# Kernel tuning notes

Hardware: AMD Instinct MI355X
Metric: run time of the kernel (lower is better)

The kernel has to match this reference:

```python
import jax, jax.numpy as jnp
import numpy as np
import math

B, T, D = 4, 2048, 1024
NHEAD = 16
HEAD_DIM = D // NHEAD
MAX_REL = 16  # max_relative_position default


def setup_inputs() -> dict:
    key = jax.random.key(0)
    ks = jax.random.split(key, 10)
    s = 1.0 / math.sqrt(D)
    inp = {
        "x": jax.random.normal(ks[0], (B, T, D), dtype=jnp.float32),
        "Wq": jax.random.normal(ks[1], (D, D), dtype=jnp.float32) * s,
        "bq": jnp.zeros((D,), dtype=jnp.float32),
        "Wk": jax.random.normal(ks[2], (D, D), dtype=jnp.float32) * s,
        "bk": jnp.zeros((D,), dtype=jnp.float32),
        "Wv": jax.random.normal(ks[3], (D, D), dtype=jnp.float32) * s,
        "bv": jnp.zeros((D,), dtype=jnp.float32),
        "rel_bias": jax.random.normal(ks[4], (2 * MAX_REL - 1, NHEAD), dtype=jnp.float32) * 0.02,
        "Wo": jax.random.normal(ks[5], (D, D), dtype=jnp.float32) * s,
        "bo": jnp.zeros((D,), dtype=jnp.float32),
    }
    return inp


def _relative_bias(rel_bias, seq_len):
    # distance matrix clamped to [-(MAX_REL-1), MAX_REL-1], shifted to index table
    r = jnp.arange(seq_len)
    dist = jnp.clip(r[None, :] - r[:, None], -MAX_REL + 1, MAX_REL - 1) + MAX_REL - 1
    # gather: [T, T, H] -> [H, T, T]
    return jnp.transpose(rel_bias[dist], (2, 0, 1))


def reference(x, Wq, bq, Wk, bk, Wv, bv, rel_bias, Wo, bo):
    Bdim, Tdim, Ddim = x.shape
    # torch Linear: x @ W.T + b
    Q = x @ Wq.T + bq
    K = x @ Wk.T + bk
    V = x @ Wv.T + bv
    # [B, H, T, hd]
    Q = Q.reshape(Bdim, Tdim, NHEAD, HEAD_DIM).transpose(0, 2, 1, 3)
    K = K.reshape(Bdim, Tdim, NHEAD, HEAD_DIM).transpose(0, 2, 1, 3)
    V = V.reshape(Bdim, Tdim, NHEAD, HEAD_DIM).transpose(0, 2, 1, 3)
    scores = jnp.einsum("bhqd,bhkd->bhqk", Q, K) / math.sqrt(HEAD_DIM)
    scores = scores + _relative_bias(rel_bias, Tdim)[None]  # [1,H,T,T]
    attn = jax.nn.softmax(scores, axis=-1)
    out = jnp.einsum("bhqk,bhkd->bhqd", attn, V)
    out = out.transpose(0, 2, 1, 3).reshape(Bdim, Tdim, Ddim)
    return out @ Wo.T + bo
```

## Files before the change

kernel.cpp:

```cpp
#include <hip/hip_runtime.h>
#include <stdint.h>
#include <math.h>

typedef unsigned short u16;
typedef __bf16 bf16x8 __attribute__((ext_vector_type(8)));
typedef float f32x4 __attribute__((ext_vector_type(4)));
typedef float f32x2 __attribute__((ext_vector_type(2)));
typedef unsigned short u16x8 __attribute__((ext_vector_type(8)));
typedef unsigned short u16x4 __attribute__((ext_vector_type(4)));

#define BATCH 4
#define SEQT 2048
#define DMODEL 1024
#define NHEAD 16
#define HDIM 64
#define LOG2E 1.44269504f

#define LDS_GLD16(gp, lp)                                                     \
  __builtin_amdgcn_global_load_lds(                                           \
      (const __attribute__((address_space(1))) void*)(gp),                    \
      (__attribute__((address_space(3))) void*)(lp), 16, 0, 0)

static __device__ __forceinline__ u16 f2bf(float f) {
  union { float f; uint32_t u; } c; c.f = f;
  uint32_t u = c.u;
  return (u16)((u + 0x7fffu + ((u >> 16) & 1u)) >> 16);
}
static __device__ __forceinline__ u16 f2bf_fast(float f) {
  union { float f; uint32_t u; } c; c.f = f;
  return (u16)((c.u + 0x8000u) >> 16);
}
static __device__ __forceinline__ uint32_t pkbf(float a, float b) {
  union { float f; uint32_t u; } ca, cb; ca.f = a; cb.f = b;
  return __builtin_amdgcn_perm(cb.u + 0x8000u, ca.u + 0x8000u, 0x07060302u);
}

__global__ __launch_bounds__(256) void k_convert_all(
    const float* __restrict__ x, const float* __restrict__ Wq,
    const float* __restrict__ Wk, const float* __restrict__ Wv,
    const float* __restrict__ Wo, u16* __restrict__ xbf,
    u16* __restrict__ Wqkv, u16* __restrict__ Wob) {
  const int NX4 = 2097152, NW4 = 262144;
  int i = blockIdx.x * 256 + threadIdx.x;
  const float* s; u16* d; int js, jd;
  if (i < NX4) {
    s = x; d = xbf; js = jd = i;
  } else if (i < NX4 + 3 * NW4) {
    int j = i - NX4;
    int w = j >> 18;
    s = (w == 0) ? Wq : (w == 1) ? Wk : Wv;
    js = j & (NW4 - 1);
    d = Wqkv; jd = j;
  } else {
    s = Wo; d = Wob; js = jd = i - NX4 - 3 * NW4;
  }
  float4 v = ((const float4*)s)[js];
  u16x4 o = {f2bf(v.x), f2bf(v.y), f2bf(v.z), f2bf(v.w)};
  ((u16x4*)d)[jd] = o;
}

__global__ __launch_bounds__(256) void k_gemm_qk(
    const u16* __restrict__ A, const u16* __restrict__ Bqk,
    const float* __restrict__ bq_, const float* __restrict__ bk_,
    u16* __restrict__ dq, u16* __restrict__ dk) {
  __shared__ u16 As[128 * 64];
  __shared__ u16 Bs[128 * 64];

  const int tid = threadIdx.x;
  const int wave = tid >> 6, lane = tid & 63;
  const int quad = lane >> 4, l16 = lane & 15;
  const int wm = wave & 1, wn = wave >> 1;
  const int m0 = blockIdx.x * 128, n0 = blockIdx.y * 128;
  const int lrow = lane >> 3, lcol = (lane & 7) * 8;

  f32x4 acc[4][4] = {};

  for (int kt = 0; kt < 1024; kt += 64) {
    __syncthreads();
    for (int c = 0; c < 4; ++c) {
      int rr = (wave * 4 + c) * 8 + lrow;
      LDS_GLD16(A + (size_t)(m0 + rr) * 1024 + kt + lcol,
                &As[(wave * 4 + c) * 512]);
      LDS_GLD16(Bqk + (size_t)(n0 + rr) * 1024 + kt + lcol,
                &Bs[(wave * 4 + c) * 512]);
    }
    __syncthreads();
    for (int kh = 0; kh < 2; ++kh) {
      bf16x8 af[4], bfr[4];
      for (int mt = 0; mt < 4; ++mt)
        af[mt] = *(const bf16x8*)&As[(wm * 64 + mt * 16 + l16) * 64 + kh * 32 +
                                     quad * 8];
      for (int nt = 0; nt < 4; ++nt)
        bfr[nt] = *(const bf16x8*)&Bs[(wn * 64 + nt * 16 + l16) * 64 + kh * 32 +
                                      quad * 8];
      for (int mt = 0; mt < 4; ++mt)
        for (int nt = 0; nt < 4; ++nt)
          acc[mt][nt] = __builtin_amdgcn_mfma_f32_16x16x32_bf16(
              af[mt], bfr[nt], acc[mt][nt], 0, 0, 0);
    }
  }

  u16* dst = (n0 < 1024) ? dq : dk;
  const float* bias = (n0 < 1024) ? bq_ : bk_;
  for (int mt = 0; mt < 4; ++mt)
    for (int nt = 0; nt < 4; ++nt) {
      int nn = (n0 + wn * 64 + nt * 16 + l16) & 1023;
      float bv = bias[nn];
      int h = nn >> 6, hd = nn & 63;
      for (int r = 0; r < 4; ++r) {
        int m = m0 + wm * 64 + mt * 16 + quad * 4 + r;
        int b = m >> 11, t = m & 2047;
        dst[(((size_t)b * NHEAD + h) * SEQT + t) * HDIM + hd] =
            f2bf_fast(acc[mt][nt][r] + bv);
      }
    }
}

__global__ __launch_bounds__(256) void k_gemm_vt(const u16* __restrict__ A,
                                                 const u16* __restrict__ Bx,
                                                 const float* __restrict__ bv_,
                                                 u16* __restrict__ Vt) {
  __shared__ u16 As[128 * 64];
  __shared__ u16 Bs[128 * 64];
  __shared__ float biasS[128];

  const int tid = threadIdx.x;
  const int wave = tid >> 6, lane = tid & 63;
  const int quad = lane >> 4, l16 = lane & 15;
  const int wm = wave & 1, wn = wave >> 1;
  const int m0 = blockIdx.x * 128, n0 = blockIdx.y * 128;
  const int lrow = lane >> 3, lcol = (lane & 7) * 8;

  if (tid < 128) biasS[tid] = bv_[m0 + tid];

  f32x4 acc[4][4] = {};

  for (int kt = 0; kt < 1024; kt += 64) {
    __syncthreads();
    for (int c = 0; c < 4; ++c) {
      int rr = (wave * 4 + c) * 8 + lrow;
      LDS_GLD16(A + (size_t)(m0 + rr) * 1024 + kt + lcol,
                &As[(wave * 4 + c) * 512]);
      LDS_GLD16(Bx + (size_t)(n0 + rr) * 1024 + kt + lcol,
                &Bs[(wave * 4 + c) * 512]);
    }
    __syncthreads();
    for (int kh = 0; kh < 2; ++kh) {
      bf16x8 af[4], bfr[4];
      for (int mt = 0; mt < 4; ++mt)
        af[mt] = *(const bf16x8*)&As[(wm * 64 + mt * 16 + l16) * 64 + kh * 32 +
                                     quad * 8];
      for (int nt = 0; nt < 4; ++nt)
        bfr[nt] = *(const bf16x8*)&Bs[(wn * 64 + nt * 16 + l16) * 64 + kh * 32 +
                                      quad * 8];
      for (int mt = 0; mt < 4; ++mt)
        for (int nt = 0; nt < 4; ++nt)
          acc[mt][nt] = __builtin_amdgcn_mfma_f32_16x16x32_bf16(
              af[mt], bfr[nt], acc[mt][nt], 0, 0, 0);
    }
  }

  for (int mt = 0; mt < 4; ++mt)
    for (int nt = 0; nt < 4; ++nt) {
      int n = n0 + wn * 64 + nt * 16 + l16;
      int b = n >> 11, t = n & 2047;
      for (int r = 0; r < 4; ++r) {
        int m = m0 + wm * 64 + mt * 16 + quad * 4 + r;
        float v = acc[mt][nt][r] + biasS[m - m0];
        Vt[((size_t)(b * NHEAD + (m >> 6)) * HDIM + (m & 63)) * SEQT + t] =
            f2bf_fast(v);
      }
    }
}

__global__ __launch_bounds__(256) void k_gemm_proj(const u16* __restrict__ A,
                                                   const u16* __restrict__ Bm,
                                                   const float* __restrict__ bias,
                                                   float* __restrict__ out) {
  __shared__ u16 As[128 * 64];
  __shared__ u16 Bs[128 * 64];

  const int tid = threadIdx.x;
  const int wave = tid >> 6, lane = tid & 63;
  const int quad = lane >> 4, l16 = lane & 15;
  const int wm = wave & 1, wn = wave >> 1;
  const int m0 = blockIdx.x * 128, n0 = blockIdx.y * 128;
  const int lrow = lane >> 3, lcol = (lane & 7) * 8;

  f32x4 acc[4][4] = {};

  for (int kt = 0; kt < 1024; kt += 64) {
    __syncthreads();
    for (int c = 0; c < 4; ++c) {
      int rr = (wave * 4 + c) * 8 + lrow;
      LDS_GLD16(A + (size_t)(m0 + rr) * 1024 + kt + lcol,
                &As[(wave * 4 + c) * 512]);
      LDS_GLD16(Bm + (size_t)(n0 + rr) * 1024 + kt + lcol,
                &Bs[(wave * 4 + c) * 512]);
    }
    __syncthreads();
    for (int kh = 0; kh < 2; ++kh) {
      bf16x8 af[4], bfr[4];
      for (int mt = 0; mt < 4; ++mt)
        af[mt] = *(const bf16x8*)&As[(wm * 64 + mt * 16 + l16) * 64 + kh * 32 +
                                     quad * 8];
      for (int nt = 0; nt < 4; ++nt)
        bfr[nt] = *(const bf16x8*)&Bs[(wn * 64 + nt * 16 + l16) * 64 + kh * 32 +
                                      quad * 8];
      for (int mt = 0; mt < 4; ++mt)
        for (int nt = 0; nt < 4; ++nt)
          acc[mt][nt] = __builtin_amdgcn_mfma_f32_16x16x32_bf16(
              af[mt], bfr[nt], acc[mt][nt], 0, 0, 0);
    }
  }

  for (int mt = 0; mt < 4; ++mt)
    for (int nt = 0; nt < 4; ++nt) {
      int n = n0 + wn * 64 + nt * 16 + l16;
      float bv = bias[n];
      for (int r = 0; r < 4; ++r) {
        int m = m0 + wm * 64 + mt * 16 + quad * 4 + r;
        out[(size_t)m * 1024 + n] = acc[mt][nt][r] + bv;
      }
    }
}

__global__ __launch_bounds__(512, 8) void k_attn(const u16* __restrict__ Qb,
                                                 const u16* __restrict__ Kb,
                                                 const u16* __restrict__ Vt,
                                                 const float* __restrict__ relb,
                                                 u16* __restrict__ Obf) {
  __shared__ u16 Ks[64 * 64];
  __shared__ u16 VTs[64 * 64];
  __shared__ u16 Ps[8][16 * 72];
  __shared__ float biasL[32];

  const int tid = threadIdx.x;
  const int wave = tid >> 6, lane = tid & 63;
  const int quad = lane >> 4, l16 = lane & 15;
  const int qt = blockIdx.x;
  const int bh = blockIdx.y;
  const int h = bh & (NHEAD - 1);
  const size_t base = (size_t)bh * SEQT * HDIM;
  const int q0 = qt * 128;
  const int qa = q0 + wave * 16;

  if (tid < 31) biasL[tid] = relb[tid * NHEAD + h] * LOG2E;
  const float bLo = relb[0 * NHEAD + h] * LOG2E;
  const float bHi = relb[30 * NHEAD + h] * LOG2E;
  const float CL = 0.125f * LOG2E;

  bf16x8 bq0, bq1;
  {
    const u16* qp = Qb + base + (size_t)(qa + l16) * HDIM;
    bq0 = *(const bf16x8*)(qp + quad * 8);
    bq1 = *(const bf16x8*)(qp + 32 + quad * 8);
  }

  f32x4 Oacc[4] = {};
  f32x2 ls2 = {};

  const int rl = lane >> 3;
  const int gb = (lane & 7) ^ rl;
  const int srow = wave * 8 + rl;
  const u16* kgp = Kb + base + (size_t)srow * HDIM + gb * 8;
  const u16* vgp = Vt + base + (size_t)srow * SEQT + gb * 8;
  u16* ksl = &Ks[wave * 512];
  u16* vsl = &VTs[wave * 512];
  const int sl = l16 & 7;

  for (int kt2 = 0; kt2 < 32; ++kt2) {
    const int k0 = kt2 * 64;
    __syncthreads();
    LDS_GLD16(kgp + (size_t)k0 * HDIM, ksl);
    LDS_GLD16(vgp + k0, vsl);
    __syncthreads();

    for (int kg = 0; kg < 4; ++kg) {
      const int krow = kg * 16 + l16;
      bf16x8 ak0 = *(const bf16x8*)&Ks[krow * 64 + ((quad ^ sl) << 3)];
      bf16x8 ak1 = *(const bf16x8*)&Ks[krow * 64 + (((4 + quad) ^ sl) << 3)];
      f32x4 s = {};
      s = __builtin_amdgcn_mfma_f32_16x16x32_bf16(ak0, bq0, s, 0, 0, 0);
      s = __builtin_amdgcn_mfma_f32_16x16x32_bf16(ak1, bq1, s, 0, 0, 0);
      const int kb = k0 + kg * 16;
      float p0, p1, p2, p3;
      const int dmin = kb - (qa + 15);
      const int dmax = kb + 15 - qa;
      if (dmin >= 15 || dmax <= -15) {
        const float ub = (dmin >= 15) ? bHi : bLo;
        p0 = __builtin_amdgcn_exp2f(fmaf(s[0], CL, ub));
        p1 = __builtin_amdgcn_exp2f(fmaf(s[1], CL, ub));
        p2 = __builtin_amdgcn_exp2f(fmaf(s[2], CL, ub));
        p3 = __builtin_amdgcn_exp2f(fmaf(s[3], CL, ub));
      } else {
        const int db = kb + quad * 4 - (qa + l16);
        float pv[4];
        for (int r = 0; r < 4; ++r) {
          int d = db + r;
          d = d < -15 ? -15 : (d > 15 ? 15 : d);
          pv[r] = __builtin_amdgcn_exp2f(fmaf(s[r], CL, biasL[d + 15]));
        }
        p0 = pv[0]; p1 = pv[1]; p2 = pv[2]; p3 = pv[3];
      }
      f32x2 t01 = {p0, p1}, t23 = {p2, p3};
      ls2 += t01 + t23;
      uint2 w;
      w.x = pkbf(p0, p1);
      w.y = pkbf(p2, p3);
      *(uint2*)&Ps[wave][l16 * 72 + kg * 16 + quad * 4] = w;
    }

    bf16x8 bp0 = *(const bf16x8*)&Ps[wave][l16 * 72 + quad * 8];
    bf16x8 bp1 = *(const bf16x8*)&Ps[wave][l16 * 72 + 32 + quad * 8];
    for (int dg = 0; dg < 4; ++dg) {
      const int d = dg * 16 + l16;
      bf16x8 av0 = *(const bf16x8*)&VTs[d * 64 + ((quad ^ sl) << 3)];
      bf16x8 av1 = *(const bf16x8*)&VTs[d * 64 + (((4 + quad) ^ sl) << 3)];
      Oacc[dg] = __builtin_amdgcn_mfma_f32_16x16x32_bf16(av0, bp0, Oacc[dg], 0, 0, 0);
      Oacc[dg] = __builtin_amdgcn_mfma_f32_16x16x32_bf16(av1, bp1, Oacc[dg], 0, 0, 0);
    }
  }

  float v = ls2.x + ls2.y;
  v += __shfl_xor(v, 16, 64);
  v += __shfl_xor(v, 32, 64);
  const float rinv = 1.0f / v;

  const int b = bh >> 4;
  const int t = qa + l16;
  u16* op = Obf + ((size_t)(b * SEQT + t)) * DMODEL + h * HDIM;
  for (int dg = 0; dg < 4; ++dg) {
    uint2 w;
    w.x = pkbf(Oacc[dg][0] * rinv, Oacc[dg][1] * rinv);
    w.y = pkbf(Oacc[dg][2] * rinv, Oacc[dg][3] * rinv);
    *(uint2*)(op + dg * 16 + quad * 4) = w;
  }
}

extern "C" void kernel_launch(void* const* d_in, const int* in_sizes, int n_in,
                              void* d_out, int out_size, void* d_ws,
                              size_t ws_size, hipStream_t stream) {
  const float* x = (const float*)d_in[0];
  const float* Wq = (const float*)d_in[1];
  const float* bq = (const float*)d_in[2];
  const float* Wk = (const float*)d_in[3];
  const float* bk = (const float*)d_in[4];
  const float* Wv = (const float*)d_in[5];
  const float* bv = (const float*)d_in[6];
  const float* relb = (const float*)d_in[7];
  const float* Wo = (const float*)d_in[8];
  const float* bo = (const float*)d_in[9];
  float* out = (float*)d_out;

  char* ws = (char*)d_ws;
  const size_t SZ_X = (size_t)BATCH * SEQT * DMODEL * 2;
  const size_t SZ_W = (size_t)DMODEL * DMODEL * 2;
  u16* xbf = (u16*)(ws);
  u16* Wqb = (u16*)(ws + SZ_X);
  u16* Wvb = (u16*)(ws + SZ_X + 2 * SZ_W);
  u16* Wob = (u16*)(ws + SZ_X + 3 * SZ_W);
  u16* Qb = (u16*)(ws + SZ_X + 4 * SZ_W);
  u16* Kb = (u16*)(ws + 2 * SZ_X + 4 * SZ_W);
  u16* Vt = (u16*)(ws + 3 * SZ_X + 4 * SZ_W);
  u16* Obf = (u16*)(ws + 4 * SZ_X + 4 * SZ_W);

  k_convert_all<<<12288, 256, 0, stream>>>(x, Wq, Wk, Wv, Wo, xbf, Wqb, Wob);
  k_gemm_qk<<<dim3(64, 16), 256, 0, stream>>>(xbf, Wqb, bq, bk, Qb, Kb);
  k_gemm_vt<<<dim3(8, 64), 256, 0, stream>>>(Wvb, xbf, bv, Vt);
  k_attn<<<dim3(16, 64), 512, 0, stream>>>(Qb, Kb, Vt, relb, Obf);
  k_gemm_proj<<<dim3(64, 8), 256, 0, stream>>>(Obf, Wob, bo, out);
}
```

Before: 323.1 us.

## Switch attention to 32x32x16 MFMA and keep P in registers

```diff
diff --git a/kernel.cpp b/kernel.cpp
--- a/kernel.cpp
+++ b/kernel.cpp
@@ -5,7 +5,7 @@
 typedef unsigned short u16;
 typedef __bf16 bf16x8 __attribute__((ext_vector_type(8)));
 typedef float f32x4 __attribute__((ext_vector_type(4)));
-typedef float f32x2 __attribute__((ext_vector_type(2)));
+typedef float f32x16 __attribute__((ext_vector_type(16)));
 typedef unsigned short u16x8 __attribute__((ext_vector_type(8)));
 typedef unsigned short u16x4 __attribute__((ext_vector_type(4)));
 
@@ -33,6 +33,12 @@
 static __device__ __forceinline__ uint32_t pkbf(float a, float b) {
   union { float f; uint32_t u; } ca, cb; ca.f = a; cb.f = b;
   return __builtin_amdgcn_perm(cb.u + 0x8000u, ca.u + 0x8000u, 0x07060302u);
+}
+static __device__ __forceinline__ bf16x8 mk_bf8(uint32_t x0, uint32_t x1,
+                                                uint32_t x2, uint32_t x3) {
+  union { uint32_t u[4]; bf16x8 v; } t;
+  t.u[0] = x0; t.u[1] = x1; t.u[2] = x2; t.u[3] = x3;
+  return t.v;
 }
 
 __global__ __launch_bounds__(256) void k_convert_all(
@@ -225,117 +231,123 @@
     }
 }
 
-__global__ __launch_bounds__(512, 8) void k_attn(const u16* __restrict__ Qb,
+__global__ __launch_bounds__(256, 4) void k_attn(const u16* __restrict__ Qb,
                                                  const u16* __restrict__ Kb,
                                                  const u16* __restrict__ Vt,
                                                  const float* __restrict__ relb,
                                                  u16* __restrict__ Obf) {
   __shared__ u16 Ks[64 * 64];
   __shared__ u16 VTs[64 * 64];
-  __shared__ u16 Ps[8][16 * 72];
   __shared__ float biasL[32];
 
   const int tid = threadIdx.x;
   const int wave = tid >> 6, lane = tid & 63;
-  const int quad = lane >> 4, l16 = lane & 15;
+  const int l32 = lane & 31, hi = lane >> 5;
   const int qt = blockIdx.x;
   const int bh = blockIdx.y;
   const int h = bh & (NHEAD - 1);
   const size_t base = (size_t)bh * SEQT * HDIM;
-  const int q0 = qt * 128;
-  const int qa = q0 + wave * 16;
+  const int qa = qt * 128 + wave * 32;
 
   if (tid < 31) biasL[tid] = relb[tid * NHEAD + h] * LOG2E;
   const float bLo = relb[0 * NHEAD + h] * LOG2E;
   const float bHi = relb[30 * NHEAD + h] * LOG2E;
   const float CL = 0.125f * LOG2E;
 
-  bf16x8 bq0, bq1;
+  bf16x8 bq[4];
   {
-    const u16* qp = Qb + base + (size_t)(qa + l16) * HDIM;
-    bq0 = *(const bf16x8*)(qp + quad * 8);
-    bq1 = *(const bf16x8*)(qp + 32 + quad * 8);
-  }
-
-  f32x4 Oacc[4] = {};
-  f32x2 ls2 = {};
-
-  const int rl = lane >> 3;
-  const int gb = (lane & 7) ^ rl;
-  const int srow = wave * 8 + rl;
-  const u16* kgp = Kb + base + (size_t)srow * HDIM + gb * 8;
-  const u16* vgp = Vt + base + (size_t)srow * SEQT + gb * 8;
-  u16* ksl = &Ks[wave * 512];
-  u16* vsl = &VTs[wave * 512];
-  const int sl = l16 & 7;
+    const u16* qp = Qb + base + (size_t)(qa + l32) * HDIM + hi * 8;
+    for (int ds = 0; ds < 4; ++ds) bq[ds] = *(const bf16x8*)(qp + ds * 16);
+  }
+
+  f32x16 Oacc[2] = {};
+  float ls = 0.f;
+
+  const int rl = lane >> 3, gb = lane & 7;
+  const int row0 = wave * 8 + rl, row1 = row0 + 32;
+  const u16* kgp0 = Kb + base + (size_t)row0 * HDIM + ((gb ^ (row0 & 7)) << 3);
+  const u16* kgp1 = Kb + base + (size_t)row1 * HDIM + ((gb ^ (row1 & 7)) << 3);
+  const u16* vgp0 = Vt + base + (size_t)row0 * SEQT + ((gb ^ (row0 & 7)) << 3);
+  const u16* vgp1 = Vt + base + (size_t)row1 * SEQT + ((gb ^ (row1 & 7)) << 3);
+  u16* ksl0 = &Ks[wave * 512 + lane * 8];
+  u16* ksl1 = ksl0 + 2048;
+  u16* vsl0 = &VTs[wave * 512 + lane * 8];
+  u16* vsl1 = vsl0 + 2048;
 
   for (int kt2 = 0; kt2 < 32; ++kt2) {
     const int k0 = kt2 * 64;
     __syncthreads();
-    LDS_GLD16(kgp + (size_t)k0 * HDIM, ksl);
-    LDS_GLD16(vgp + k0, vsl);
-    __syncthreads();
-
-    for (int kg = 0; kg < 4; ++kg) {
-      const int krow = kg * 16 + l16;
-      bf16x8 ak0 = *(const bf16x8*)&Ks[krow * 64 + ((quad ^ sl) << 3)];
-      bf16x8 ak1 = *(const bf16x8*)&Ks[krow * 64 + (((4 + quad) ^ sl) << 3)];
-      f32x4 s = {};
-      s = __builtin_amdgcn_mfma_f32_16x16x32_bf16(ak0, bq0, s, 0, 0, 0);
-      s = __builtin_amdgcn_mfma_f32_16x16x32_bf16(ak1, bq1, s, 0, 0, 0);
-      const int kb = k0 + kg * 16;
-      float p0, p1, p2, p3;
-      const int dmin = kb - (qa + 15);
-      const int dmax = kb + 15 - qa;
-      if (dmin >= 15 || dmax <= -15) {
+    LDS_GLD16(kgp0 + (size_t)k0 * HDIM, ksl0);
+    LDS_GLD16(kgp1 + (size_t)k0 * HDIM, ksl1);
+    LDS_GLD16(vgp0 + k0, vsl0);
+    LDS_GLD16(vgp1 + k0, vsl1);
+    __syncthreads();
+
+    for (int kgrp = 0; kgrp < 2; ++kgrp) {
+      const int kb = k0 + kgrp * 32;
+      f32x16 c = {};
+      for (int ds = 0; ds < 4; ++ds) {
+        const int key = kgrp * 32 + l32;
+        bf16x8 ak = *(const bf16x8*)&Ks[key * 64 +
+                                        (((ds * 2 + hi) ^ (key & 7)) << 3)];
+        c = __builtin_amdgcn_mfma_f32_32x32x16_bf16(ak, bq[ds], c, 0, 0, 0);
+      }
+
+      const int dmin = kb - (qa + 31);
+      if (dmin >= 15 || kb + 31 - qa <= -15) {
         const float ub = (dmin >= 15) ? bHi : bLo;
-        p0 = __builtin_amdgcn_exp2f(fmaf(s[0], CL, ub));
-        p1 = __builtin_amdgcn_exp2f(fmaf(s[1], CL, ub));
-        p2 = __builtin_amdgcn_exp2f(fmaf(s[2], CL, ub));
-        p3 = __builtin_amdgcn_exp2f(fmaf(s[3], CL, ub));
+        for (int i = 0; i < 16; ++i)
+          c[i] = __builtin_amdgcn_exp2f(fmaf(c[i], CL, ub));
       } else {
-        const int db = kb + quad * 4 - (qa + l16);
-        float pv[4];
-        for (int r = 0; r < 4; ++r) {
-          int d = db + r;
+        const int dbase = kb + 4 * hi - (qa + l32);
+        for (int i = 0; i < 16; ++i) {
+          int d = dbase + (i & 3) + 8 * (i >> 2);
           d = d < -15 ? -15 : (d > 15 ? 15 : d);
-          pv[r] = __builtin_amdgcn_exp2f(fmaf(s[r], CL, biasL[d + 15]));
+          c[i] = __builtin_amdgcn_exp2f(fmaf(c[i], CL, biasL[d + 15]));
         }
-        p0 = pv[0]; p1 = pv[1]; p2 = pv[2]; p3 = pv[3];
-      }
-      f32x2 t01 = {p0, p1}, t23 = {p2, p3};
-      ls2 += t01 + t23;
+      }
+      {
+        float s0 = (c[0] + c[1]) + (c[2] + c[3]);
+        float s1 = (c[4] + c[5]) + (c[6] + c[7]);
+        float s2 = (c[8] + c[9]) + (c[10] + c[11]);
+        float s3 = (c[12] + c[13]) + (c[14] + c[15]);
+        ls += (s0 + s1) + (s2 + s3);
+      }
+
+      uint32_t p[8];
+      for (int i = 0; i < 8; ++i) p[i] = pkbf(c[2 * i], c[2 * i + 1]);
+
+      for (int ks = 0; ks < 2; ++ks) {
+        bf16x8 bp = mk_bf8(p[ks * 4 + 0], p[ks * 4 + 1], p[ks * 4 + 2],
+                           p[ks * 4 + 3]);
+        const int blk = kgrp * 4 + ks * 2;
+        for (int dg = 0; dg < 2; ++dg) {
+          const int d = dg * 32 + l32;
+          const int sw = d & 7;
+          uint2 a0 = *(const uint2*)&VTs[d * 64 + ((blk ^ sw) << 3) + 4 * hi];
+          uint2 a1 =
+              *(const uint2*)&VTs[d * 64 + (((blk + 1) ^ sw) << 3) + 4 * hi];
+          bf16x8 av = mk_bf8(a0.x, a0.y, a1.x, a1.y);
+          Oacc[dg] = __builtin_amdgcn_mfma_f32_32x32x16_bf16(av, bp, Oacc[dg],
+                                                             0, 0, 0);
+        }
+      }
+    }
+  }
+
+  ls += __shfl_xor(ls, 32, 64);
+  const float rinv = 1.0f / ls;
+
+  const int b = bh >> 4;
+  const int t = qa + l32;
+  u16* op = Obf + ((size_t)(b * SEQT + t)) * DMODEL + h * HDIM;
+  for (int dg = 0; dg < 2; ++dg)
+    for (int a = 0; a < 4; ++a) {
       uint2 w;
-      w.x = pkbf(p0, p1);
-      w.y = pkbf(p2, p3);
-      *(uint2*)&Ps[wave][l16 * 72 + kg * 16 + quad * 4] = w;
-    }
-
-    bf16x8 bp0 = *(const bf16x8*)&Ps[wave][l16 * 72 + quad * 8];
-    bf16x8 bp1 = *(const bf16x8*)&Ps[wave][l16 * 72 + 32 + quad * 8];
-    for (int dg = 0; dg < 4; ++dg) {
-      const int d = dg * 16 + l16;
-      bf16x8 av0 = *(const bf16x8*)&VTs[d * 64 + ((quad ^ sl) << 3)];
-      bf16x8 av1 = *(const bf16x8*)&VTs[d * 64 + (((4 + quad) ^ sl) << 3)];
-      Oacc[dg] = __builtin_amdgcn_mfma_f32_16x16x32_bf16(av0, bp0, Oacc[dg], 0, 0, 0);
-      Oacc[dg] = __builtin_amdgcn_mfma_f32_16x16x32_bf16(av1, bp1, Oacc[dg], 0, 0, 0);
-    }
-  }
-
-  float v = ls2.x + ls2.y;
-  v += __shfl_xor(v, 16, 64);
-  v += __shfl_xor(v, 32, 64);
-  const float rinv = 1.0f / v;
-
-  const int b = bh >> 4;
-  const int t = qa + l16;
-  u16* op = Obf + ((size_t)(b * SEQT + t)) * DMODEL + h * HDIM;
-  for (int dg = 0; dg < 4; ++dg) {
-    uint2 w;
-    w.x = pkbf(Oacc[dg][0] * rinv, Oacc[dg][1] * rinv);
-    w.y = pkbf(Oacc[dg][2] * rinv, Oacc[dg][3] * rinv);
-    *(uint2*)(op + dg * 16 + quad * 4) = w;
-  }
+      w.x = pkbf(Oacc[dg][4 * a + 0] * rinv, Oacc[dg][4 * a + 1] * rinv);
+      w.y = pkbf(Oacc[dg][4 * a + 2] * rinv, Oacc[dg][4 * a + 3] * rinv);
+      *(uint2*)(op + dg * 32 + 8 * a + 4 * hi) = w;
+    }
 }
 
 extern "C" void kernel_launch(void* const* d_in, const int* in_sizes, int n_in,
@@ -368,6 +380,6 @@
   k_convert_all<<<12288, 256, 0, stream>>>(x, Wq, Wk, Wv, Wo, xbf, Wqb, Wob);
   k_gemm_qk<<<dim3(64, 16), 256, 0, stream>>>(xbf, Wqb, bq, bk, Qb, Kb);
   k_gemm_vt<<<dim3(8, 64), 256, 0, stream>>>(Wvb, xbf, bv, Vt);
-  k_attn<<<dim3(16, 64), 512, 0, stream>>>(Qb, Kb, Vt, relb, Obf);
+  k_attn<<<dim3(16, 64), 256, 0, stream>>>(Qb, Kb, Vt, relb, Obf);
   k_gemm_proj<<<dim3(64, 8), 256, 0, stream>>>(Obf, Wob, bo, out);
 }
```

New measurement: 316.2 us. -2.1%, faster.
